# Optimization experiments

Measured on AMD Instinct MI355X. Metric: run time of the kernel, lower is better.

Reference implementation:

```python
import jax, jax.numpy as jnp
import numpy as np

EPSILON = 1e-8
NUM_STEPS = 1000
S_OFFSET = 0.0001
POWER = 2
CLIPMAX = 0.999
B = 1048576


def _schedule():
    t = jnp.arange(0, NUM_STEPS + 1, dtype=jnp.float32)
    f_t = jnp.cos(np.pi / 2 * (t / NUM_STEPS + S_OFFSET) / (1 + S_OFFSET)) ** POWER
    alpha_bars = f_t / f_t[0]
    betas = jnp.concatenate([jnp.zeros([1], jnp.float32), 1.0 - alpha_bars[1:] / alpha_bars[:-1]])
    betas = jnp.minimum(betas, CLIPMAX)
    sigmas = jnp.sqrt(betas[1:] * ((1.0 - alpha_bars[:-1]) / (1.0 - alpha_bars[1:])))
    sigmas = jnp.concatenate([jnp.zeros([1], jnp.float32), sigmas])
    return alpha_bars, betas, sigmas


def setup_inputs() -> dict:
    key = jax.random.key(0)
    k1, k2, k3, k4, k5 = jax.random.split(key, 5)
    lt = jax.random.normal(k1, (B, 6), dtype=jnp.float32)
    predicted_l0 = jax.random.normal(k2, (B, 6), dtype=jnp.float32)
    pred_lattice = jax.random.normal(k3, (B, 3, 3), dtype=jnp.float32)
    z_noise = jax.random.normal(k4, (B, 6), dtype=jnp.float32)  # torch.randn_like(lt), frozen
    t = jax.random.randint(k5, (B,), 0, NUM_STEPS, dtype=jnp.int64)
    alpha_bars, betas, sigmas = _schedule()
    return {
        "lt": lt,
        "predicted_l0": predicted_l0,
        "pred_lattice": pred_lattice,
        "alpha_bars": alpha_bars,
        "betas": betas,
        "sigmas": sigmas,
        "z_noise": z_noise,
        "t": t,
    }


def reference(lt, predicted_l0, pred_lattice, alpha_bars, betas, sigmas, z_noise, t):
    # VP_lattice.reverse
    alpha = 1.0 - betas[t]
    alpha = jnp.maximum(alpha, 1.0 - betas[-2])  # clamp_min
    alpha_bar = alpha_bars[t]
    sigma = sigmas[t][:, None]

    # polar_decomposition: only the symmetric factor L_tilda = V diag(S) V^T is used
    _, S, Vt = jnp.linalg.svd(pred_lattice, full_matrices=False)  # (B,3),(B,3,3)
    L = jnp.einsum("bji,bj,bjk->bik", Vt, S, Vt)  # Vt^T @ diag(S) @ Vt
    L = (L + jnp.swapaxes(L, 1, 2)) / 2  # symmetrize

    # symmetric_matrix_to_vector: upper triangular incl. diagonal
    vec = jnp.stack([L[:, 0, 0], L[:, 0, 1], L[:, 0, 2], L[:, 1, 1], L[:, 1, 2], L[:, 2, 2]], axis=1)

    predicted_noise = lt - (vec + predicted_l0) / 2
    z = jnp.where((t > 1)[:, None], z_noise, jnp.zeros_like(z_noise))
    coef = (1.0 / jnp.sqrt(alpha + EPSILON))[:, None]
    scale = ((1.0 - alpha) / jnp.sqrt(1.0 - alpha_bar + EPSILON))[:, None]
    return coef * (lt - scale * predicted_noise) + sigma * z
```

## Files before the change

### kernel.cpp

```cpp
#include <hip/hip_runtime.h>


#define NUM_STEPS 1000
#define TBL 1008
#define BLOCK 256

__global__ __launch_bounds__(256) void sched_kernel(
    const float* __restrict__ alpha_bars,
    const float* __restrict__ betas,
    const float* __restrict__ sigmas,
    float* __restrict__ ws)
{
    int j = blockIdx.x * blockDim.x + threadIdx.x;
    if (j >= TBL) return;
    if (j <= NUM_STEPS) {
        float beta_last = betas[NUM_STEPS - 1];
        float alpha = 1.0f - fminf(betas[j], beta_last);
        float coef  = 1.0f / sqrtf(alpha + 1e-8f);
        float scale = (1.0f - alpha) / sqrtf(1.0f - alpha_bars[j] + 1e-8f);
        ws[j]           = coef * (1.0f - scale);
        ws[TBL + j]     = 0.5f * coef * scale;
        ws[2 * TBL + j] = (j > 1) ? sigmas[j] : 0.0f;
    } else {
        ws[j] = 0.0f; ws[TBL + j] = 0.0f; ws[2 * TBL + j] = 0.0f;
    }
}

__global__ __launch_bounds__(BLOCK) void vp_lattice_kernel(
    const float* __restrict__ lt,
    const float* __restrict__ pl0,
    const float* __restrict__ plat,
    const float* __restrict__ alpha_bars,
    const float* __restrict__ betas,
    const float* __restrict__ sigmas,
    const float* __restrict__ z_noise,
    const int*   __restrict__ t,
    float* __restrict__ out,
    int n,
    const float* __restrict__ ws,
    int use_ws)
{
    __shared__ __align__(16) float sA[TBL];
    __shared__ __align__(16) float sB[TBL];
    __shared__ __align__(16) float sS[TBL];
    __shared__ __align__(16) float platT[BLOCK * 9];

    const int tid = threadIdx.x;
    const int rowBase = blockIdx.x * BLOCK;
    int rem = n - rowBase; if (rem > BLOCK) rem = BLOCK;
    const bool full = (rem == BLOCK);

    if (full) {
        const float4* g9 = reinterpret_cast<const float4*>(plat + (size_t)rowBase * 9);
        float4*       s9 = reinterpret_cast<float4*>(platT);
#pragma unroll
        for (int k = 0; k < 3; ++k) {
            int j = tid + k * BLOCK;
            if (j < BLOCK * 9 / 4) s9[j] = g9[j];
        }
    } else {
        for (int j = tid; j < rem * 9; j += BLOCK)
            platT[j] = plat[(size_t)rowBase * 9 + j];
    }

    if (use_ws) {
        const float4* w4 = reinterpret_cast<const float4*>(ws);
        float4* a4 = reinterpret_cast<float4*>(sA);
        float4* b4 = reinterpret_cast<float4*>(sB);
        float4* s4 = reinterpret_cast<float4*>(sS);
        for (int j = tid; j < TBL / 4; j += BLOCK) {
            a4[j] = w4[j];
            b4[j] = w4[TBL / 4 + j];
            s4[j] = w4[2 * (TBL / 4) + j];
        }
    } else {
        float beta_last = betas[NUM_STEPS - 1];
        for (int j = tid; j < TBL; j += BLOCK) {
            float A = 0.0f, Bc = 0.0f, S = 0.0f;
            if (j <= NUM_STEPS) {
                float alpha = 1.0f - fminf(betas[j], beta_last);
                float coef  = 1.0f / sqrtf(alpha + 1e-8f);
                float scale = (1.0f - alpha) / sqrtf(1.0f - alpha_bars[j] + 1e-8f);
                A  = coef * (1.0f - scale);
                Bc = 0.5f * coef * scale;
                S  = (j > 1) ? sigmas[j] : 0.0f;
            }
            sA[j] = A; sB[j] = Bc; sS[j] = S;
        }
    }

    int ti = (tid < rem) ? t[rowBase + tid] : 0;

    __syncthreads();

    if (tid >= rem) return;

    size_t b6 = (size_t)(rowBase + tid) * 6;
    const float2* lt2 = reinterpret_cast<const float2*>(lt + b6);
    const float2* p02 = reinterpret_cast<const float2*>(pl0 + b6);
    const float2* zn2 = reinterpret_cast<const float2*>(z_noise + b6);
    float2 lw0 = lt2[0], lw1 = lt2[1], lw2 = lt2[2];
    float2 pw0 = p02[0], pw1 = p02[1], pw2 = p02[2];
    float2 zw0 = zn2[0], zw1 = zn2[1], zw2 = zn2[2];

    float A  = sA[ti];
    float Bc = sB[ti];
    float S  = sS[ti];

    const float* pr = platT + tid * 9;
    float a00 = pr[0], a01 = pr[1], a02 = pr[2];
    float a10 = pr[3], a11 = pr[4], a12 = pr[5];
    float a20 = pr[6], a21 = pr[7], a22 = pr[8];

    float m00 = a00*a00 + a10*a10 + a20*a20;
    float m01 = a00*a01 + a10*a11 + a20*a21;
    float m02 = a00*a02 + a10*a12 + a20*a22;
    float m11 = a01*a01 + a11*a11 + a21*a21;
    float m12 = a01*a02 + a11*a12 + a21*a22;
    float m22 = a02*a02 + a12*a12 + a22*a22;

    float q  = (m00 + m11 + m22) * (1.0f/3.0f);
    float b00 = m00 - q, b11 = m11 - q, b22 = m22 - q;
    float p1 = m01*m01 + m02*m02 + m12*m12;
    float p2 = b00*b00 + b11*b11 + b22*b22 + 2.0f*p1;
    float p  = sqrtf(p2 * (1.0f/6.0f));
    float detB = b00*(b11*b22 - m12*m12)
               - m01*(m01*b22 - m12*m02)
               + m02*(m01*m12 - b11*m02);
    float pinv = __fdividef(1.0f, fmaxf(p, 1e-20f));
    float r = 0.5f * detB * pinv * pinv * pinv;
    r = fminf(fmaxf(r, -1.0f), 1.0f);

    float ar = fabsf(r);
    float sq = sqrtf(1.0f - ar);
    float pl = 1.5707288f + ar * (-0.2121144f + ar * (0.0742610f - ar * 0.0187293f));
    float ac = sq * pl;
    float acr = (r >= 0.0f) ? ac : (3.14159265358979f - ac);
    float phi = acr * (1.0f/3.0f);
    float mu1 = q + 2.0f*p*__cosf(phi);
    float mu3 = q + 2.0f*p*__cosf(phi + 2.0943951023931953f);
    float mu2 = 3.0f*q - mu1 - mu3;
    float l1 = sqrtf(fmaxf(mu1, 0.0f));
    float l2 = sqrtf(fmaxf(mu2, 0.0f));
    float l3 = sqrtf(fmaxf(mu3, 0.0f));

    float IU   = l1 + l2 + l3;
    float IIU  = l1*(l2 + l3) + l2*l3;
    float IIIU = l1*l2*l3;
    float denom = (l1 + l2) * (l1 + l3) * (l2 + l3);
    float dinv  = __fdividef(1.0f, fmaxf(denom, 1e-25f));
    float sd = (IU*IU - IIU) * dinv;
    float td = IU * IIIU * dinv;
    float nd = -dinv;

    float mm00 = m00*m00 + m01*m01 + m02*m02;
    float mm01 = m00*m01 + m01*m11 + m02*m12;
    float mm02 = m00*m02 + m01*m12 + m02*m22;
    float mm11 = m01*m01 + m11*m11 + m12*m12;
    float mm12 = m01*m02 + m11*m12 + m12*m22;
    float mm22 = m02*m02 + m12*m12 + m22*m22;

    float v0 = nd*mm00 + sd*m00 + td;
    float v1 = nd*mm01 + sd*m01;
    float v2 = nd*mm02 + sd*m02;
    float v3 = nd*mm11 + sd*m11 + td;
    float v4 = nd*mm12 + sd*m12;
    float v5 = nd*mm22 + sd*m22 + td;

    float2 o0, o1, o2;
    o0.x = A*lw0.x + Bc*(v0 + pw0.x) + S*zw0.x;
    o0.y = A*lw0.y + Bc*(v1 + pw0.y) + S*zw0.y;
    o1.x = A*lw1.x + Bc*(v2 + pw1.x) + S*zw1.x;
    o1.y = A*lw1.y + Bc*(v3 + pw1.y) + S*zw1.y;
    o2.x = A*lw2.x + Bc*(v4 + pw2.x) + S*zw2.x;
    o2.y = A*lw2.y + Bc*(v5 + pw2.y) + S*zw2.y;

    float2* out2 = reinterpret_cast<float2*>(out + b6);
    out2[0] = o0;
    out2[1] = o1;
    out2[2] = o2;
}

extern "C" void kernel_launch(void* const* d_in, const int* in_sizes, int n_in,
                              void* d_out, int out_size, void* d_ws, size_t ws_size,
                              hipStream_t stream) {
    const float* lt         = (const float*)d_in[0];
    const float* pl0        = (const float*)d_in[1];
    const float* plat       = (const float*)d_in[2];
    const float* alpha_bars = (const float*)d_in[3];
    const float* betas      = (const float*)d_in[4];
    const float* sigmas     = (const float*)d_in[5];
    const float* z_noise    = (const float*)d_in[6];
    const int*   t          = (const int*)d_in[7];
    float* out = (float*)d_out;
    float* ws  = (float*)d_ws;

    int n = in_sizes[0] / 6;
    int use_ws = (ws != nullptr && ws_size >= (size_t)(3 * TBL * sizeof(float)));

    if (use_ws) {
        sched_kernel<<<(TBL + 255) / 256, 256, 0, stream>>>(alpha_bars, betas, sigmas, ws);
    }
    int grid = (n + BLOCK - 1) / BLOCK;
    vp_lattice_kernel<<<grid, BLOCK, 0, stream>>>(
        lt, pl0, plat, alpha_bars, betas, sigmas, z_noise, t, out, n, ws, use_ws);
}
```

Measured before the change: 153.7 us.

## Stage all row data through per-wave LDS with coalesced vector loads and stores

Each wave now loads its 64 rows of lattice, lt, pl0 and z_noise with fully coalesced float4/float2 loads into a per-wave shared-memory staging area. Outputs are staged back through LDS and written out coalesced. Each block also handles two tiles of 256 rows, which halves the number of blocks and spreads the per-block schedule-table setup over more rows. In exchange, LDS use and the number of LDS transactions rise, and the strided per-lane LDS reads may cause bank conflicts, which could lower occupancy.

```diff
diff --git a/kernel.cpp b/kernel.cpp
--- a/kernel.cpp
+++ b/kernel.cpp
@@ -4,6 +4,15 @@
 #define NUM_STEPS 1000
 #define TBL 1008
 #define BLOCK 256
+#define WAVES 4
+#define TILES 2
+#define RPB (BLOCK * TILES)
+
+#define W_PLAT 0
+#define W_LT   576
+#define W_PL0  960
+#define W_ZN   1344
+#define W_SZ   1728
 
 __global__ __launch_bounds__(256) void sched_kernel(
     const float* __restrict__ alpha_bars,
@@ -26,6 +35,69 @@
     }
 }
 
+__device__ __forceinline__ void sqrtm_vec(const float* __restrict__ pr,
+                                          float vv[6])
+{
+    float a00 = pr[0], a01 = pr[1], a02 = pr[2];
+    float a10 = pr[3], a11 = pr[4], a12 = pr[5];
+    float a20 = pr[6], a21 = pr[7], a22 = pr[8];
+
+    float m00 = a00*a00 + a10*a10 + a20*a20;
+    float m01 = a00*a01 + a10*a11 + a20*a21;
+    float m02 = a00*a02 + a10*a12 + a20*a22;
+    float m11 = a01*a01 + a11*a11 + a21*a21;
+    float m12 = a01*a02 + a11*a12 + a21*a22;
+    float m22 = a02*a02 + a12*a12 + a22*a22;
+
+    float q  = (m00 + m11 + m22) * (1.0f/3.0f);
+    float b00 = m00 - q, b11 = m11 - q, b22 = m22 - q;
+    float p1 = m01*m01 + m02*m02 + m12*m12;
+    float p2 = b00*b00 + b11*b11 + b22*b22 + 2.0f*p1;
+    float p  = sqrtf(p2 * (1.0f/6.0f));
+    float detB = b00*(b11*b22 - m12*m12)
+               - m01*(m01*b22 - m12*m02)
+               + m02*(m01*m12 - b11*m02);
+    float pinv = __fdividef(1.0f, fmaxf(p, 1e-20f));
+    float r = 0.5f * detB * pinv * pinv * pinv;
+    r = fminf(fmaxf(r, -1.0f), 1.0f);
+
+    float ar = fabsf(r);
+    float sq = sqrtf(1.0f - ar);
+    float pl = 1.5707288f + ar * (-0.2121144f + ar * (0.0742610f - ar * 0.0187293f));
+    float ac = sq * pl;
+    float acr = (r >= 0.0f) ? ac : (3.14159265358979f - ac);
+    float phi = acr * (1.0f/3.0f);
+    float mu1 = q + 2.0f*p*__cosf(phi);
+    float mu3 = q + 2.0f*p*__cosf(phi + 2.0943951023931953f);
+    float mu2 = 3.0f*q - mu1 - mu3;
+    float l1 = sqrtf(fmaxf(mu1, 0.0f));
+    float l2 = sqrtf(fmaxf(mu2, 0.0f));
+    float l3 = sqrtf(fmaxf(mu3, 0.0f));
+
+    float IU   = l1 + l2 + l3;
+    float IIU  = l1*(l2 + l3) + l2*l3;
+    float IIIU = l1*l2*l3;
+    float denom = (l1 + l2) * (l1 + l3) * (l2 + l3);
+    float dinv  = __fdividef(1.0f, fmaxf(denom, 1e-25f));
+    float sd = (IU*IU - IIU) * dinv;
+    float td = IU * IIIU * dinv;
+    float nd = -dinv;
+
+    float mm00 = m00*m00 + m01*m01 + m02*m02;
+    float mm01 = m00*m01 + m01*m11 + m02*m12;
+    float mm02 = m00*m02 + m01*m12 + m02*m22;
+    float mm11 = m01*m01 + m11*m11 + m12*m12;
+    float mm12 = m01*m02 + m11*m12 + m12*m22;
+    float mm22 = m02*m02 + m12*m12 + m22*m22;
+
+    vv[0] = nd*mm00 + sd*m00 + td;
+    vv[1] = nd*mm01 + sd*m01;
+    vv[2] = nd*mm02 + sd*m02;
+    vv[3] = nd*mm11 + sd*m11 + td;
+    vv[4] = nd*mm12 + sd*m12;
+    vv[5] = nd*mm22 + sd*m22 + td;
+}
+
 __global__ __launch_bounds__(BLOCK) void vp_lattice_kernel(
     const float* __restrict__ lt,
     const float* __restrict__ pl0,
@@ -43,25 +115,12 @@
     __shared__ __align__(16) float sA[TBL];
     __shared__ __align__(16) float sB[TBL];
     __shared__ __align__(16) float sS[TBL];
-    __shared__ __align__(16) float platT[BLOCK * 9];
-
-    const int tid = threadIdx.x;
-    const int rowBase = blockIdx.x * BLOCK;
-    int rem = n - rowBase; if (rem > BLOCK) rem = BLOCK;
-    const bool full = (rem == BLOCK);
-
-    if (full) {
-        const float4* g9 = reinterpret_cast<const float4*>(plat + (size_t)rowBase * 9);
-        float4*       s9 = reinterpret_cast<float4*>(platT);
-#pragma unroll
-        for (int k = 0; k < 3; ++k) {
-            int j = tid + k * BLOCK;
-            if (j < BLOCK * 9 / 4) s9[j] = g9[j];
-        }
-    } else {
-        for (int j = tid; j < rem * 9; j += BLOCK)
-            platT[j] = plat[(size_t)rowBase * 9 + j];
-    }
+    __shared__ __align__(16) float sW[WAVES * W_SZ];
+
+    const int tid  = threadIdx.x;
+    const int lane = tid & 63;
+    const int wv   = tid >> 6;
+    const int rowBase = blockIdx.x * RPB;
 
     if (use_ws) {
         const float4* w4 = reinterpret_cast<const float4*>(ws);
@@ -88,97 +147,90 @@
             sA[j] = A; sB[j] = Bc; sS[j] = S;
         }
     }
-
-    int ti = (tid < rem) ? t[rowBase + tid] : 0;
-
     __syncthreads();
 
-    if (tid >= rem) return;
-
-    size_t b6 = (size_t)(rowBase + tid) * 6;
-    const float2* lt2 = reinterpret_cast<const float2*>(lt + b6);
-    const float2* p02 = reinterpret_cast<const float2*>(pl0 + b6);
-    const float2* zn2 = reinterpret_cast<const float2*>(z_noise + b6);
-    float2 lw0 = lt2[0], lw1 = lt2[1], lw2 = lt2[2];
-    float2 pw0 = p02[0], pw1 = p02[1], pw2 = p02[2];
-    float2 zw0 = zn2[0], zw1 = zn2[1], zw2 = zn2[2];
-
-    float A  = sA[ti];
-    float Bc = sB[ti];
-    float S  = sS[ti];
-
-    const float* pr = platT + tid * 9;
-    float a00 = pr[0], a01 = pr[1], a02 = pr[2];
-    float a10 = pr[3], a11 = pr[4], a12 = pr[5];
-    float a20 = pr[6], a21 = pr[7], a22 = pr[8];
-
-    float m00 = a00*a00 + a10*a10 + a20*a20;
-    float m01 = a00*a01 + a10*a11 + a20*a21;
-    float m02 = a00*a02 + a10*a12 + a20*a22;
-    float m11 = a01*a01 + a11*a11 + a21*a21;
-    float m12 = a01*a02 + a11*a12 + a21*a22;
-    float m22 = a02*a02 + a12*a12 + a22*a22;
-
-    float q  = (m00 + m11 + m22) * (1.0f/3.0f);
-    float b00 = m00 - q, b11 = m11 - q, b22 = m22 - q;
-    float p1 = m01*m01 + m02*m02 + m12*m12;
-    float p2 = b00*b00 + b11*b11 + b22*b22 + 2.0f*p1;
-    float p  = sqrtf(p2 * (1.0f/6.0f));
-    float detB = b00*(b11*b22 - m12*m12)
-               - m01*(m01*b22 - m12*m02)
-               + m02*(m01*m12 - b11*m02);
-    float pinv = __fdividef(1.0f, fmaxf(p, 1e-20f));
-    float r = 0.5f * detB * pinv * pinv * pinv;
-    r = fminf(fmaxf(r, -1.0f), 1.0f);
-
-    float ar = fabsf(r);
-    float sq = sqrtf(1.0f - ar);
-    float pl = 1.5707288f + ar * (-0.2121144f + ar * (0.0742610f - ar * 0.0187293f));
-    float ac = sq * pl;
-    float acr = (r >= 0.0f) ? ac : (3.14159265358979f - ac);
-    float phi = acr * (1.0f/3.0f);
-    float mu1 = q + 2.0f*p*__cosf(phi);
-    float mu3 = q + 2.0f*p*__cosf(phi + 2.0943951023931953f);
-    float mu2 = 3.0f*q - mu1 - mu3;
-    float l1 = sqrtf(fmaxf(mu1, 0.0f));
-    float l2 = sqrtf(fmaxf(mu2, 0.0f));
-    float l3 = sqrtf(fmaxf(mu3, 0.0f));
-
-    float IU   = l1 + l2 + l3;
-    float IIU  = l1*(l2 + l3) + l2*l3;
-    float IIIU = l1*l2*l3;
-    float denom = (l1 + l2) * (l1 + l3) * (l2 + l3);
-    float dinv  = __fdividef(1.0f, fmaxf(denom, 1e-25f));
-    float sd = (IU*IU - IIU) * dinv;
-    float td = IU * IIIU * dinv;
-    float nd = -dinv;
-
-    float mm00 = m00*m00 + m01*m01 + m02*m02;
-    float mm01 = m00*m01 + m01*m11 + m02*m12;
-    float mm02 = m00*m02 + m01*m12 + m02*m22;
-    float mm11 = m01*m01 + m11*m11 + m12*m12;
-    float mm12 = m01*m02 + m11*m12 + m12*m22;
-    float mm22 = m02*m02 + m12*m12 + m22*m22;
-
-    float v0 = nd*mm00 + sd*m00 + td;
-    float v1 = nd*mm01 + sd*m01;
-    float v2 = nd*mm02 + sd*m02;
-    float v3 = nd*mm11 + sd*m11 + td;
-    float v4 = nd*mm12 + sd*m12;
-    float v5 = nd*mm22 + sd*m22 + td;
-
-    float2 o0, o1, o2;
-    o0.x = A*lw0.x + Bc*(v0 + pw0.x) + S*zw0.x;
-    o0.y = A*lw0.y + Bc*(v1 + pw0.y) + S*zw0.y;
-    o1.x = A*lw1.x + Bc*(v2 + pw1.x) + S*zw1.x;
-    o1.y = A*lw1.y + Bc*(v3 + pw1.y) + S*zw1.y;
-    o2.x = A*lw2.x + Bc*(v4 + pw2.x) + S*zw2.x;
-    o2.y = A*lw2.y + Bc*(v5 + pw2.y) + S*zw2.y;
-
-    float2* out2 = reinterpret_cast<float2*>(out + b6);
-    out2[0] = o0;
-    out2[1] = o1;
-    out2[2] = o2;
+    float* w = sW + wv * W_SZ;
+
+#pragma unroll
+    for (int tile = 0; tile < TILES; ++tile) {
+        const int rowW = rowBase + tile * BLOCK + wv * 64;
+
+        if (rowW + 64 <= n) {
+            const float* gP = plat    + (size_t)rowW * 9;
+            const float* gL = lt      + (size_t)rowW * 6;
+            const float* gQ = pl0     + (size_t)rowW * 6;
+            const float* gZ = z_noise + (size_t)rowW * 6;
+
+            float4 pA = reinterpret_cast<const float4*>(gP)[lane];
+            float4 pB = reinterpret_cast<const float4*>(gP)[64 + lane];
+            float  pC = gP[512 + lane];
+            float4 lA = reinterpret_cast<const float4*>(gL)[lane];
+            float2 lB = reinterpret_cast<const float2*>(gL + 256)[lane];
+            float4 qA = reinterpret_cast<const float4*>(gQ)[lane];
+            float2 qB = reinterpret_cast<const float2*>(gQ + 256)[lane];
+            float4 zA = reinterpret_cast<const float4*>(gZ)[lane];
+            float2 zB = reinterpret_cast<const float2*>(gZ + 256)[lane];
+            int ti = t[rowW + lane];
+
+            reinterpret_cast<float4*>(w + W_PLAT)[lane]      = pA;
+            reinterpret_cast<float4*>(w + W_PLAT)[64 + lane] = pB;
+            w[W_PLAT + 512 + lane]                           = pC;
+            reinterpret_cast<float4*>(w + W_LT)[lane]        = lA;
+            reinterpret_cast<float2*>(w + W_LT + 256)[lane]  = lB;
+            reinterpret_cast<float4*>(w + W_PL0)[lane]       = qA;
+            reinterpret_cast<float2*>(w + W_PL0 + 256)[lane] = qB;
+            reinterpret_cast<float4*>(w + W_ZN)[lane]        = zA;
+            reinterpret_cast<float2*>(w + W_ZN + 256)[lane]  = zB;
+
+            float va[6];
+            sqrtm_vec(w + W_PLAT + lane * 9, va);
+
+            float A  = sA[ti];
+            float Bc = sB[ti];
+            float S  = sS[ti];
+
+            const float* lr = w + W_LT  + lane * 6;
+            const float* qr = w + W_PL0 + lane * 6;
+            const float* zr = w + W_ZN  + lane * 6;
+
+            float o[6];
+#pragma unroll
+            for (int c = 0; c < 6; ++c) {
+                float lc = lr[c];
+                o[c] = A * lc + Bc * (va[c] + qr[c]) + S * zr[c];
+            }
+
+            float2* ow = reinterpret_cast<float2*>(w + W_PLAT);
+            ow[lane * 3 + 0] = make_float2(o[0], o[1]);
+            ow[lane * 3 + 1] = make_float2(o[2], o[3]);
+            ow[lane * 3 + 2] = make_float2(o[4], o[5]);
+
+            float* oG = out + (size_t)rowW * 6;
+            reinterpret_cast<float4*>(oG)[lane] =
+                reinterpret_cast<const float4*>(w + W_PLAT)[lane];
+            reinterpret_cast<float2*>(oG + 256)[lane] =
+                reinterpret_cast<const float2*>(w + W_PLAT + 256)[lane];
+        } else {
+            int row = rowW + lane;
+            if (row < n) {
+                float ab[9];
+#pragma unroll
+                for (int k = 0; k < 9; ++k) ab[k] = plat[(size_t)row * 9 + k];
+                float va[6];
+                sqrtm_vec(ab, va);
+                int ti = t[row];
+                float A  = sA[ti];
+                float Bc = sB[ti];
+                float S  = sS[ti];
+                size_t b6 = (size_t)row * 6;
+#pragma unroll
+                for (int c = 0; c < 6; ++c) {
+                    float lc = lt[b6 + c];
+                    out[b6 + c] = A * lc + Bc * (va[c] + pl0[b6 + c]) + S * z_noise[b6 + c];
+                }
+            }
+        }
+    }
 }
 
 extern "C" void kernel_launch(void* const* d_in, const int* in_sizes, int n_in,
@@ -201,7 +253,7 @@
     if (use_ws) {
         sched_kernel<<<(TBL + 255) / 256, 256, 0, stream>>>(alpha_bars, betas, sigmas, ws);
     }
-    int grid = (n + BLOCK - 1) / BLOCK;
+    int grid = (n + RPB - 1) / RPB;
     vp_lattice_kernel<<<grid, BLOCK, 0, stream>>>(
         lt, pl0, plat, alpha_bars, betas, sigmas, z_noise, t, out, n, ws, use_ws);
 }
```

After: 157.0 us. 2.2% more time.
